# Performance work log

Measured on AMD Instinct MI355X. Metric: run time of the kernel, lower is better.

## Reference

```python
import jax, jax.numpy as jnp
import numpy as np

B, N, H, F = 4, 4096, 128, 64
ADJ_DENSITY = 0.01


def setup_inputs() -> dict:
    key = jax.random.key(0)
    k1, k2, k3, k4, k5 = jax.random.split(key, 5)
    x = jax.random.normal(k1, (B, N, H), dtype=jnp.float32)
    w_scale = jnp.float32(1.0 / np.sqrt(H))  # ~ nn.Linear init scale
    Wq = jax.random.normal(k2, (H, F), dtype=jnp.float32) * w_scale
    Wk = jax.random.normal(k3, (H, F), dtype=jnp.float32) * w_scale
    Wv = jax.random.normal(k4, (H, F), dtype=jnp.float32) * w_scale
    # Sparse binary adjacency with self-loops (every row has >=1 neighbor,
    # so no all--inf softmax rows).
    adj = (jax.random.uniform(k5, (N, N)) < ADJ_DENSITY).astype(jnp.float32)
    diag = jnp.arange(N)
    adj = adj.at[diag, diag].set(1.0)
    return {"x": x, "Wq": Wq, "Wk": Wk, "Wv": Wv, "adj": adj}


def reference(x, Wq, Wk, Wv, adj):
    # x: (B,N,H); Wq/Wk/Wv: (H,F); adj: (N,N) binary, broadcast over batch.
    q = x @ Wq  # (B,N,F)
    k = x @ Wk  # (B,N,F)
    v = x @ Wv  # (B,N,F)
    scale = jnp.float32(F) ** -0.5  # k.shape[-1] ** -0.5
    scores = jnp.einsum("bnf,bmf->bnm", q, k) * scale  # (B,N,N)
    scores = jnp.where(adj[None] == 0, -jnp.inf, scores)
    # softmax over neighbors, then the module adds the adjacency back (wei + adj)
    wei = jax.nn.softmax(scores, axis=-1) + adj[None]  # (B,N,N)
    # dropout is identity in eval/deterministic reference
    out = jnp.einsum("bnm,bmf->bnf", wei, v)  # (B,N,F)
    return out
```

## Files before the change

### kernel.cpp

```cpp
#include <hip/hip_runtime.h>
#include <math.h>

#define Bb 4
#define Nn 4096
#define Hh 128
#define Ff 64
#define NBR_CAP 192

typedef __attribute__((ext_vector_type(8))) short bf16x8;
typedef __attribute__((ext_vector_type(4))) float f32x4;

__device__ __forceinline__ unsigned short f2bf(float f) {
  unsigned int u = __float_as_uint(f);
  u += 0x7fffu + ((u >> 16) & 1u);
  return (unsigned short)(u >> 16);
}
__device__ __forceinline__ float bf2f(unsigned short h) {
  return __uint_as_float(((unsigned int)h) << 16);
}

__global__ __launch_bounds__(256) void qkv_kernel(
    const float* __restrict__ x,
    const float* __restrict__ Wq,
    const float* __restrict__ Wk,
    const float* __restrict__ Wv,
    float* __restrict__ q,
    unsigned short* __restrict__ kb,
    unsigned short* __restrict__ vb) {
  __shared__ short xs[64 * 128];

  const int tid = threadIdx.x;
  const int w = tid >> 6;
  const int lane = tid & 63;

  const int row0 = (int)blockIdx.x * 64;
  const int half = lane >> 4;
  const int l16 = lane & 15;

  const float4* xg = (const float4*)(x + (size_t)row0 * Hh);
#pragma unroll
  for (int j = 0; j < 8; ++j) {
    const int idx = tid + 256 * j;
    const int row = idx >> 5;
    const int c4 = idx & 31;
    const float4 xv = xg[idx];
    uint2 p;
    p.x = (unsigned)f2bf(xv.x) | ((unsigned)f2bf(xv.y) << 16);
    p.y = (unsigned)f2bf(xv.z) | ((unsigned)f2bf(xv.w) << 16);
    const int addr = (row * 256 + c4 * 8) ^ ((row & 7) << 4);
    *(uint2*)((char*)xs + addr) = p;
  }

  bf16x8 bfr[3][4];
#pragma unroll
  for (int nt = 0; nt < 3; ++nt) {
    const int n0g = w * 48 + nt * 16;
    const float* Wm = (n0g < 64) ? Wq : (n0g < 128) ? Wk : Wv;
    const int c0 = n0g & 63;
#pragma unroll
    for (int ks = 0; ks < 4; ++ks) {
      bf16x8 f;
#pragma unroll
      for (int j = 0; j < 8; ++j) {
        const int kr = ks * 32 + half * 8 + j;
        f[j] = (short)f2bf(Wm[kr * Ff + c0 + l16]);
      }
      bfr[nt][ks] = f;
    }
  }
  __syncthreads();

  f32x4 acc[4][3];
#pragma unroll
  for (int mt = 0; mt < 4; ++mt)
#pragma unroll
    for (int nt = 0; nt < 3; ++nt)
#pragma unroll
      for (int r = 0; r < 4; ++r) acc[mt][nt][r] = 0.f;

#pragma unroll
  for (int mt = 0; mt < 4; ++mt) {
    const int arow = mt * 16 + l16;
    const int abase = arow * 256;
    const int aswz = (arow & 7) << 4;
#pragma unroll
    for (int ks = 0; ks < 4; ++ks) {
      const int addr = (abase + ks * 64 + half * 16) ^ aswz;
      const bf16x8 a = *(const bf16x8*)((const char*)xs + addr);
#pragma unroll
      for (int nt = 0; nt < 3; ++nt) {
        acc[mt][nt] = __builtin_amdgcn_mfma_f32_16x16x32_bf16(
            a, bfr[nt][ks], acc[mt][nt], 0, 0, 0);
      }
    }
  }

#pragma unroll
  for (int mt = 0; mt < 4; ++mt) {
#pragma unroll
    for (int nt = 0; nt < 3; ++nt) {
      const int n0g = w * 48 + nt * 16;
      const int col = (n0g & 63) + l16;
#pragma unroll
      for (int r = 0; r < 4; ++r) {
        const size_t rowg = (size_t)row0 + mt * 16 + half * 4 + r;
        const float val = acc[mt][nt][r];
        if (n0g < 64)
          q[rowg * Ff + col] = val;
        else if (n0g < 128)
          kb[rowg * Ff + col] = f2bf(val);
        else
          vb[rowg * Ff + col] = f2bf(val);
      }
    }
  }
}

__global__ __launch_bounds__(256) void attn_kernel(
    const float* __restrict__ adj,
    const float* __restrict__ q,
    const unsigned short* __restrict__ kb,
    const unsigned short* __restrict__ vb,
    float* __restrict__ out) {
  __shared__ __align__(8) unsigned short nbr[NBR_CAP];
  __shared__ float qs[4][64];
  __shared__ float ps[4][64];
  __shared__ int wcnt[4];

  const int n = blockIdx.x;
  const int tid = threadIdx.x;
  const int w = tid >> 6;
  const int lane = tid & 63;

  qs[w][lane] = q[((size_t)w * Nn + n) * Ff + lane];

  const float* arow = adj + (size_t)n * Nn;
  float4 a4[4];
#pragma unroll
  for (int j = 0; j < 4; ++j) a4[j] = ((const float4*)arow)[tid + 256 * j];

  int cnt = 0;
#pragma unroll
  for (int j = 0; j < 4; ++j) {
    cnt += (a4[j].x != 0.f) + (a4[j].y != 0.f) + (a4[j].z != 0.f) +
           (a4[j].w != 0.f);
  }

  int inc = cnt;
#pragma unroll
  for (int o = 1; o < 64; o <<= 1) {
    const int t = __shfl_up(inc, o, 64);
    if (lane >= o) inc += t;
  }
  if (lane == 63) wcnt[w] = inc;
  __syncthreads();

  int base = 0, tot = 0;
#pragma unroll
  for (int w2 = 0; w2 < 4; ++w2) {
    const int c = wcnt[w2];
    if (w2 < w) base += c;
    tot += c;
  }
  if (tot > NBR_CAP) tot = NBR_CAP;

  int pos = base + (inc - cnt);
#pragma unroll
  for (int j = 0; j < 4; ++j) {
    const int col0 = 4 * (tid + 256 * j);
#pragma unroll
    for (int comp = 0; comp < 4; ++comp) {
      const float val = comp == 0 ? a4[j].x
                      : comp == 1 ? a4[j].y
                      : comp == 2 ? a4[j].z
                                  : a4[j].w;
      if (val != 0.f) {
        if (pos < NBR_CAP) nbr[pos] = (unsigned short)(col0 + comp);
        ++pos;
      }
    }
  }
  __syncthreads();

  const int b = w;
  const unsigned short* kbb = kb + (size_t)b * Nn * Ff;
  const unsigned short* vbb = vb + (size_t)b * Nn * Ff;

  const int g = lane >> 2;
  const int sl = lane & 3;

  float4 q0a = *(const float4*)&qs[b][8 * sl];
  float4 q0b = *(const float4*)&qs[b][8 * sl + 4];
  float4 q1a = *(const float4*)&qs[b][32 + 8 * sl];
  float4 q1b = *(const float4*)&qs[b][32 + 8 * sl + 4];

  float M = -INFINITY, L = 0.f, acc = 0.f, vsum = 0.f;

  const int ntiles = (tot + 63) >> 6;
  for (int t = 0; t < ntiles; ++t) {
    const int tbase = t << 6;

    float s0, s1, s2, s3;
#define BPAIR(u, qlo, qhi, a)                                   \
    {                                                           \
      const float flo = __uint_as_float((u) << 16);             \
      const float fhi = __uint_as_float((u) & 0xffff0000u);     \
      a = fmaf(qlo, flo, a);                                    \
      a = fmaf(qhi, fhi, a);                                    \
    }
#define DOT_ROW(i, sdst)                                                  \
    {                                                                     \
      const int idx = tbase + g + 16 * (i);                               \
      const bool valid = idx < tot;                                       \
      const int m = valid ? (int)nbr[idx] : 0;                            \
      const char* krow = (const char*)(kbb + (size_t)m * Ff);             \
      const uint4 k0 = *(const uint4*)(krow + 16 * sl);                   \
      const uint4 k1 = *(const uint4*)(krow + 64 + 16 * sl);              \
      float a = 0.f;                                                      \
      BPAIR(k0.x, q0a.x, q0a.y, a)                                        \
      BPAIR(k0.y, q0a.z, q0a.w, a)                                        \
      BPAIR(k0.z, q0b.x, q0b.y, a)                                        \
      BPAIR(k0.w, q0b.z, q0b.w, a)                                        \
      BPAIR(k1.x, q1a.x, q1a.y, a)                                        \
      BPAIR(k1.y, q1a.z, q1a.w, a)                                        \
      BPAIR(k1.z, q1b.x, q1b.y, a)                                        \
      BPAIR(k1.w, q1b.z, q1b.w, a)                                        \
      a += __shfl_xor(a, 1, 64);                                          \
      a += __shfl_xor(a, 2, 64);                                          \
      sdst = valid ? a * 0.125f : -INFINITY;                              \
    }
    DOT_ROW(0, s0)
    DOT_ROW(1, s1)
    DOT_ROW(2, s2)
    DOT_ROW(3, s3)
#undef DOT_ROW
#undef BPAIR

    float lm = fmaxf(fmaxf(s0, s1), fmaxf(s2, s3));
#pragma unroll
    for (int o = 32; o; o >>= 1) lm = fmaxf(lm, __shfl_xor(lm, o, 64));
    const float newM = fmaxf(M, lm);

    const float p0 = (s0 == -INFINITY) ? 0.f : __expf(s0 - newM);
    const float p1 = (s1 == -INFINITY) ? 0.f : __expf(s1 - newM);
    const float p2 = (s2 == -INFINITY) ? 0.f : __expf(s2 - newM);
    const float p3 = (s3 == -INFINITY) ? 0.f : __expf(s3 - newM);

    float psum = ((p0 + p1) + (p2 + p3));
#pragma unroll
    for (int o = 32; o >= 4; o >>= 1) psum += __shfl_xor(psum, o, 64);

    const float corr = __expf(M - newM);
    L = L * corr + psum;
    acc *= corr;
    M = newM;

    const float pw = sl == 0 ? p0 : sl == 1 ? p1 : sl == 2 ? p2 : p3;
    ps[w][g + 16 * sl] = pw;

    const int jmax = min(64, tot - tbase);
#pragma unroll 4
    for (int j = 0; j < jmax; ++j) {
      const int m = nbr[tbase + j];
      const float vf = bf2f(vbb[(size_t)m * Ff + lane]);
      acc = fmaf(ps[w][j], vf, acc);
      vsum += vf;
    }
  }

  out[((size_t)b * Nn + n) * Ff + lane] = acc / L + vsum;
}

extern "C" void kernel_launch(void* const* d_in, const int* in_sizes, int n_in,
                              void* d_out, int out_size, void* d_ws, size_t ws_size,
                              hipStream_t stream) {
  const float* x = (const float*)d_in[0];
  const float* Wq = (const float*)d_in[1];
  const float* Wk = (const float*)d_in[2];
  const float* Wv = (const float*)d_in[3];
  const float* adj = (const float*)d_in[4];
  float* out = (float*)d_out;

  char* ws = (char*)d_ws;
  const size_t rows = (size_t)Bb * Nn;
  float* q = (float*)ws;
  unsigned short* kb = (unsigned short*)(ws + rows * Ff * 4);
  unsigned short* vb = (unsigned short*)(ws + rows * Ff * 4 + rows * Ff * 2);

  qkv_kernel<<<dim3(256), dim3(256), 0, stream>>>(x, Wq, Wk, Wv, q, kb, vb);
  attn_kernel<<<dim3(Nn), dim3(256), 0, stream>>>(adj, q, kb, vb, out);
}
```

Baseline: 50.06 us.

## Move adjacency neighbor-list compaction into the QKV projection kernel

Builds the per-row neighbor index lists from the dense adjacency in a combined prep kernel, whose extra blocks run alongside the QKV projection blocks. The attention kernel then loads a compact index list and count instead of scanning a 16 KB adjacency row per block. This overlaps the adjacency scan with the projection GEMM and removes the scan and block-wide prefix sum from the attention critical path. Neighbor capacity drops from 192 to 128, which silently truncates rows with more neighbors, and the compacted lists add a small workspace round trip.

```diff
diff --git a/kernel.cpp b/kernel.cpp
--- a/kernel.cpp
+++ b/kernel.cpp
@@ -5,7 +5,7 @@
 #define Nn 4096
 #define Hh 128
 #define Ff 64
-#define NBR_CAP 192
+#define CAP 128
 
 typedef __attribute__((ext_vector_type(8))) short bf16x8;
 typedef __attribute__((ext_vector_type(4))) float f32x4;
@@ -19,113 +19,169 @@
   return __uint_as_float(((unsigned int)h) << 16);
 }
 
-__global__ __launch_bounds__(256) void qkv_kernel(
+__global__ __launch_bounds__(256) void prep_kernel(
     const float* __restrict__ x,
     const float* __restrict__ Wq,
     const float* __restrict__ Wk,
     const float* __restrict__ Wv,
+    const float* __restrict__ adj,
     float* __restrict__ q,
     unsigned short* __restrict__ kb,
-    unsigned short* __restrict__ vb) {
+    unsigned short* __restrict__ vb,
+    unsigned short* __restrict__ g_nbr, int* __restrict__ g_cnt) {
   __shared__ short xs[64 * 128];
+  __shared__ __align__(8) unsigned short stg[4][2][CAP];
 
   const int tid = threadIdx.x;
   const int w = tid >> 6;
   const int lane = tid & 63;
-
-  const int row0 = (int)blockIdx.x * 64;
-  const int half = lane >> 4;
-  const int l16 = lane & 15;
-
-  const float4* xg = (const float4*)(x + (size_t)row0 * Hh);
-#pragma unroll
-  for (int j = 0; j < 8; ++j) {
-    const int idx = tid + 256 * j;
-    const int row = idx >> 5;
-    const int c4 = idx & 31;
-    const float4 xv = xg[idx];
-    uint2 p;
-    p.x = (unsigned)f2bf(xv.x) | ((unsigned)f2bf(xv.y) << 16);
-    p.y = (unsigned)f2bf(xv.z) | ((unsigned)f2bf(xv.w) << 16);
-    const int addr = (row * 256 + c4 * 8) ^ ((row & 7) << 4);
-    *(uint2*)((char*)xs + addr) = p;
-  }
-
-  bf16x8 bfr[3][4];
-#pragma unroll
-  for (int nt = 0; nt < 3; ++nt) {
-    const int n0g = w * 48 + nt * 16;
-    const float* Wm = (n0g < 64) ? Wq : (n0g < 128) ? Wk : Wv;
-    const int c0 = n0g & 63;
-#pragma unroll
-    for (int ks = 0; ks < 4; ++ks) {
-      bf16x8 f;
-#pragma unroll
-      for (int j = 0; j < 8; ++j) {
-        const int kr = ks * 32 + half * 8 + j;
-        f[j] = (short)f2bf(Wm[kr * Ff + c0 + l16]);
-      }
-      bfr[nt][ks] = f;
-    }
-  }
-  __syncthreads();
-
-  f32x4 acc[4][3];
-#pragma unroll
-  for (int mt = 0; mt < 4; ++mt)
-#pragma unroll
-    for (int nt = 0; nt < 3; ++nt)
-#pragma unroll
-      for (int r = 0; r < 4; ++r) acc[mt][nt][r] = 0.f;
-
-#pragma unroll
-  for (int mt = 0; mt < 4; ++mt) {
-    const int arow = mt * 16 + l16;
-    const int abase = arow * 256;
-    const int aswz = (arow & 7) << 4;
-#pragma unroll
-    for (int ks = 0; ks < 4; ++ks) {
-      const int addr = (abase + ks * 64 + half * 16) ^ aswz;
-      const bf16x8 a = *(const bf16x8*)((const char*)xs + addr);
-#pragma unroll
-      for (int nt = 0; nt < 3; ++nt) {
-        acc[mt][nt] = __builtin_amdgcn_mfma_f32_16x16x32_bf16(
-            a, bfr[nt][ks], acc[mt][nt], 0, 0, 0);
-      }
-    }
-  }
-
-#pragma unroll
-  for (int mt = 0; mt < 4; ++mt) {
+  const int bid = (int)blockIdx.x;
+
+  if (bid >= 256 && bid < 512) {
+    const int row0 = (bid - 256) * 64;
+    const int half = lane >> 4;
+    const int l16 = lane & 15;
+
+    const float4* xg = (const float4*)(x + (size_t)row0 * Hh);
+#pragma unroll
+    for (int j = 0; j < 8; ++j) {
+      const int idx = tid + 256 * j;
+      const int row = idx >> 5;
+      const int c4 = idx & 31;
+      const float4 xv = xg[idx];
+      uint2 p;
+      p.x = (unsigned)f2bf(xv.x) | ((unsigned)f2bf(xv.y) << 16);
+      p.y = (unsigned)f2bf(xv.z) | ((unsigned)f2bf(xv.w) << 16);
+      const int addr = (row * 256 + c4 * 8) ^ ((row & 7) << 4);
+      *(uint2*)((char*)xs + addr) = p;
+    }
+
+    bf16x8 bfr[3][4];
 #pragma unroll
     for (int nt = 0; nt < 3; ++nt) {
       const int n0g = w * 48 + nt * 16;
-      const int col = (n0g & 63) + l16;
-#pragma unroll
-      for (int r = 0; r < 4; ++r) {
-        const size_t rowg = (size_t)row0 + mt * 16 + half * 4 + r;
-        const float val = acc[mt][nt][r];
-        if (n0g < 64)
-          q[rowg * Ff + col] = val;
-        else if (n0g < 128)
-          kb[rowg * Ff + col] = f2bf(val);
-        else
-          vb[rowg * Ff + col] = f2bf(val);
-      }
+      const float* Wm = (n0g < 64) ? Wq : (n0g < 128) ? Wk : Wv;
+      const int c0 = n0g & 63;
+#pragma unroll
+      for (int ks = 0; ks < 4; ++ks) {
+        bf16x8 f;
+#pragma unroll
+        for (int j = 0; j < 8; ++j) {
+          const int kr = ks * 32 + half * 8 + j;
+          f[j] = (short)f2bf(Wm[kr * Ff + c0 + l16]);
+        }
+        bfr[nt][ks] = f;
+      }
+    }
+    __syncthreads();
+
+    f32x4 acc[4][3];
+#pragma unroll
+    for (int mt = 0; mt < 4; ++mt)
+#pragma unroll
+      for (int nt = 0; nt < 3; ++nt)
+#pragma unroll
+        for (int r = 0; r < 4; ++r) acc[mt][nt][r] = 0.f;
+
+#pragma unroll
+    for (int mt = 0; mt < 4; ++mt) {
+      const int arow = mt * 16 + l16;
+      const int abase = arow * 256;
+      const int aswz = (arow & 7) << 4;
+#pragma unroll
+      for (int ks = 0; ks < 4; ++ks) {
+        const int addr = (abase + ks * 64 + half * 16) ^ aswz;
+        const bf16x8 a = *(const bf16x8*)((const char*)xs + addr);
+#pragma unroll
+        for (int nt = 0; nt < 3; ++nt) {
+          acc[mt][nt] = __builtin_amdgcn_mfma_f32_16x16x32_bf16(
+              a, bfr[nt][ks], acc[mt][nt], 0, 0, 0);
+        }
+      }
+    }
+
+#pragma unroll
+    for (int mt = 0; mt < 4; ++mt) {
+#pragma unroll
+      for (int nt = 0; nt < 3; ++nt) {
+        const int n0g = w * 48 + nt * 16;
+        const int col = (n0g & 63) + l16;
+#pragma unroll
+        for (int r = 0; r < 4; ++r) {
+          const size_t rowg = (size_t)row0 + mt * 16 + half * 4 + r;
+          const float val = acc[mt][nt][r];
+          if (n0g < 64)
+            q[rowg * Ff + col] = val;
+          else if (n0g < 128)
+            kb[rowg * Ff + col] = f2bf(val);
+          else
+            vb[rowg * Ff + col] = f2bf(val);
+        }
+      }
+    }
+  } else {
+    const int cidx = (bid < 256) ? bid : (bid - 256);
+    const int n0 = cidx * 8 + w * 2;
+
+    for (int rr = 0; rr < 2; ++rr) {
+      const int n = n0 + rr;
+      const float4* ap = (const float4*)(adj + (size_t)n * Nn);
+      unsigned short* srow = stg[w][rr];
+
+      ((ushort2*)srow)[lane] = make_ushort2(0, 0);
+
+      float4 a4[16];
+#pragma unroll
+      for (int j = 0; j < 16; ++j) a4[j] = ap[j * 64 + lane];
+
+      int cnt = 0;
+#pragma unroll
+      for (int j = 0; j < 16; ++j) {
+        cnt += (a4[j].x != 0.f) + (a4[j].y != 0.f) + (a4[j].z != 0.f) +
+               (a4[j].w != 0.f);
+      }
+
+      int inc = cnt;
+#pragma unroll
+      for (int o = 1; o < 64; o <<= 1) {
+        const int t = __shfl_up(inc, o, 64);
+        if (lane >= o) inc += t;
+      }
+
+      int pos = inc - cnt;
+#pragma unroll
+      for (int j = 0; j < 16; ++j) {
+        const int col0 = 4 * (j * 64 + lane);
+#pragma unroll
+        for (int comp = 0; comp < 4; ++comp) {
+          const float val = comp == 0 ? a4[j].x
+                          : comp == 1 ? a4[j].y
+                          : comp == 2 ? a4[j].z
+                                      : a4[j].w;
+          if (val != 0.f) {
+            if (pos < CAP) srow[pos] = (unsigned short)(col0 + comp);
+            ++pos;
+          }
+        }
+      }
+
+      const int tot = __shfl(inc, 63, 64);
+      if (lane == 0) g_cnt[n] = tot < CAP ? tot : CAP;
+      ((ushort2*)(g_nbr + (size_t)n * CAP))[lane] = ((const ushort2*)srow)[lane];
     }
   }
 }
 
 __global__ __launch_bounds__(256) void attn_kernel(
-    const float* __restrict__ adj,
+    const unsigned short* __restrict__ g_nbr,
+    const int* __restrict__ g_cnt,
     const float* __restrict__ q,
     const unsigned short* __restrict__ kb,
     const unsigned short* __restrict__ vb,
     float* __restrict__ out) {
-  __shared__ __align__(8) unsigned short nbr[NBR_CAP];
+  __shared__ __align__(8) unsigned short nbr[CAP];
   __shared__ float qs[4][64];
   __shared__ float ps[4][64];
-  __shared__ int wcnt[4];
 
   const int n = blockIdx.x;
   const int tid = threadIdx.x;
@@ -133,53 +189,10 @@
   const int lane = tid & 63;
 
   qs[w][lane] = q[((size_t)w * Nn + n) * Ff + lane];
-
-  const float* arow = adj + (size_t)n * Nn;
-  float4 a4[4];
-#pragma unroll
-  for (int j = 0; j < 4; ++j) a4[j] = ((const float4*)arow)[tid + 256 * j];
-
-  int cnt = 0;
-#pragma unroll
-  for (int j = 0; j < 4; ++j) {
-    cnt += (a4[j].x != 0.f) + (a4[j].y != 0.f) + (a4[j].z != 0.f) +
-           (a4[j].w != 0.f);
+  if (w == 0) {
+    ((ushort2*)nbr)[lane] = ((const ushort2*)(g_nbr + (size_t)n * CAP))[lane];
   }
-
-  int inc = cnt;
-#pragma unroll
-  for (int o = 1; o < 64; o <<= 1) {
-    const int t = __shfl_up(inc, o, 64);
-    if (lane >= o) inc += t;
-  }
-  if (lane == 63) wcnt[w] = inc;
-  __syncthreads();
-
-  int base = 0, tot = 0;
-#pragma unroll
-  for (int w2 = 0; w2 < 4; ++w2) {
-    const int c = wcnt[w2];
-    if (w2 < w) base += c;
-    tot += c;
-  }
-  if (tot > NBR_CAP) tot = NBR_CAP;
-
-  int pos = base + (inc - cnt);
-#pragma unroll
-  for (int j = 0; j < 4; ++j) {
-    const int col0 = 4 * (tid + 256 * j);
-#pragma unroll
-    for (int comp = 0; comp < 4; ++comp) {
-      const float val = comp == 0 ? a4[j].x
-                      : comp == 1 ? a4[j].y
-                      : comp == 2 ? a4[j].z
-                                  : a4[j].w;
-      if (val != 0.f) {
-        if (pos < NBR_CAP) nbr[pos] = (unsigned short)(col0 + comp);
-        ++pos;
-      }
-    }
-  }
+  const int tot = g_cnt[n];
   __syncthreads();
 
   const int b = w;
@@ -286,7 +299,10 @@
   float* q = (float*)ws;
   unsigned short* kb = (unsigned short*)(ws + rows * Ff * 4);
   unsigned short* vb = (unsigned short*)(ws + rows * Ff * 4 + rows * Ff * 2);
-
-  qkv_kernel<<<dim3(256), dim3(256), 0, stream>>>(x, Wq, Wk, Wv, q, kb, vb);
-  attn_kernel<<<dim3(Nn), dim3(256), 0, stream>>>(adj, q, kb, vb, out);
-}
+  unsigned short* g_nbr = (unsigned short*)(ws + rows * Ff * 8);
+  int* g_cnt = (int*)(ws + rows * Ff * 8 + (size_t)Nn * CAP * 2);
+
+  prep_kernel<<<dim3(768), dim3(256), 0, stream>>>(
+      x, Wq, Wk, Wv, adj, q, kb, vb, g_nbr, g_cnt);
+  attn_kernel<<<dim3(Nn), dim3(256), 0, stream>>>(g_nbr, g_cnt, q, kb, vb, out);
+}
```

After: 46.81 us. 1.07x faster.
